# Kernel tuning notes

Hardware: AMD Instinct MI355X
Metric: run time of the kernel (lower is better)

The kernel has to match this reference:

```python
import jax, jax.numpy as jnp
import numpy as np
import math

B, T, D = 4, 4096, 512
K_CACHE = 16

def _layernorm(x, g, b, eps=1e-5):
    mu = x.mean(-1, keepdims=True)
    var = ((x - mu) ** 2).mean(-1, keepdims=True)
    return (x - mu) / jnp.sqrt(var + eps) * g + b

def _shift1(x):
    # prepend zero along time axis, drop last: x_prev[t] = x[t-1]
    return jnp.pad(x, ((0, 0), (1, 0), (0, 0)))[:, :-1]

def mipt_parallel_scan(p, theta, inp_re, inp_im):
    # Faithful replication of the torch loop: ceil(log2(T+1)) iterations,
    # each combining with the element shifted by ONE position (as written).
    Bt, Tt, Dt = p.shape
    a_re = (1.0 - p) * jnp.cos(theta)
    a_im = (1.0 - p) * jnp.sin(theta)
    b_re, b_im = inp_re, inp_im
    mask = (jnp.arange(Tt) >= 1)[None, :, None]
    steps = math.ceil(math.log2(Tt + 1))
    for _ in range(steps):
        ar_p, ai_p = _shift1(a_re), _shift1(a_im)
        br_p, bi_p = _shift1(b_re), _shift1(b_im)
        new_a_re = a_re * ar_p - a_im * ai_p
        new_a_im = a_re * ai_p + a_im * ar_p
        new_b_re = a_re * br_p - a_im * bi_p + b_re
        new_b_im = a_re * bi_p + a_im * br_p + b_im
        a_re = jnp.where(mask, new_a_re, a_re)
        a_im = jnp.where(mask, new_a_im, a_im)
        b_re = jnp.where(mask, new_b_re, b_re)
        b_im = jnp.where(mask, new_b_im, b_im)
    return b_re, b_im

def setup_inputs() -> dict:
    key = jax.random.key(0)
    ks = jax.random.split(key, 32)
    s = 0.02
    def W(k, i, o):
        return jax.random.normal(k, (i, o), jnp.float32) * s
    inp = {
        'x': jax.random.normal(ks[0], (B, T, D), jnp.float32),
        'ln1_g': jnp.ones((D,), jnp.float32), 'ln1_b': jnp.zeros((D,), jnp.float32),
        'ln2_g': jnp.ones((D,), jnp.float32), 'ln2_b': jnp.zeros((D,), jnp.float32),
        'Wp_w': W(ks[1], D, D), 'Wp_b': jnp.zeros((D,), jnp.float32),
        'Wt_w': W(ks[2], D, D), 'Wt_b': jnp.zeros((D,), jnp.float32),
        'Wr_w': W(ks[3], D, D), 'Wr_b': jnp.zeros((D,), jnp.float32),
        'Wi_w': W(ks[4], D, D), 'Wi_b': jnp.zeros((D,), jnp.float32),
        'Wk_w': W(ks[5], D, D), 'Wk_b': jnp.zeros((D,), jnp.float32),
        'Wv_w': W(ks[6], D, D), 'Wv_b': jnp.zeros((D,), jnp.float32),
        'Wq_w': W(ks[7], D, D), 'Wq_b': jnp.zeros((D,), jnp.float32),
        'gate_w': W(ks[8], D, 1), 'gate_b': jnp.zeros((1,), jnp.float32),
        'ffn1_w': W(ks[9], D, 4 * D), 'ffn1_b': jnp.zeros((4 * D,), jnp.float32),
        'ffn2_w': W(ks[10], 4 * D, D), 'ffn2_b': jnp.zeros((D,), jnp.float32),
    }
    return inp

def reference(x, ln1_g, ln1_b, ln2_g, ln2_b, Wp_w, Wp_b, Wt_w, Wt_b, Wr_w, Wr_b,
              Wi_w, Wi_b, Wk_w, Wk_b, Wv_w, Wv_b, Wq_w, Wq_b, gate_w, gate_b,
              ffn1_w, ffn1_b, ffn2_w, ffn2_b):
    Bx, Tx, Dx = x.shape
    residual = x
    xn = _layernorm(x, ln1_g, ln1_b)
    p = jax.nn.sigmoid(xn @ Wp_w + Wp_b)
    theta = xn @ Wt_w + Wt_b
    inp_re = xn @ Wr_w + Wr_b
    inp_im = xn @ Wi_w + Wi_b
    h_re, _h_im = mipt_parallel_scan(p, theta, inp_re, inp_im)
    h_mean = h_re.mean(axis=1)  # [B, D]
    # CausalSparseCache (eval mode)
    p_scalar = p.mean(axis=-1)  # [B, T]
    K = min(K_CACHE, Tx)
    _, topk_idx = jax.lax.top_k(p_scalar, K)  # [B, K]
    idx = jnp.broadcast_to(topk_idx[:, :, None], (Bx, K, Dx))
    h_topk = jnp.take_along_axis(h_re, idx, axis=1)  # [B, K, D]
    keys = h_topk @ Wk_w + Wk_b
    values = h_topk @ Wv_w + Wv_b
    query = (h_mean @ Wq_w + Wq_b)[:, None, :]  # [B, 1, D]
    scores = jnp.einsum('bqd,bkd->bqk', query, keys) / math.sqrt(Dx)
    attn = jax.nn.softmax(scores, axis=-1)
    cache_out = jnp.einsum('bqk,bkd->bqd', attn, values)[:, 0]  # [B, D]
    g = jax.nn.sigmoid(h_mean @ gate_w + gate_b)  # [B, 1]
    out = h_mean + g * cache_out
    h = h_re + residual
    hn = _layernorm(h, ln2_g, ln2_b)
    ffn = jax.nn.gelu(hn @ ffn1_w + ffn1_b, approximate=False) @ ffn2_w + ffn2_b
    h = h + ffn
    return (h, out)
```

## Files before the change

### kernel.cpp

```cpp
#include <hip/hip_runtime.h>
#include <hip/hip_bf16.h>
#include <cstdint>
#include <cstddef>

typedef __bf16 bf16;
typedef __attribute__((ext_vector_type(8))) __bf16 bf16x8;
typedef __attribute__((ext_vector_type(4))) __bf16 bf16x4;
typedef __attribute__((ext_vector_type(4))) float f32x4;

#define BB 4
#define TT 4096
#define DD 512
#define MM (BB * TT)
#define OUT1_OFF ((size_t)MM * DD)

typedef __attribute__((address_space(1))) void as1_void;
typedef __attribute__((address_space(3))) void as3_void;

__device__ __forceinline__ void gl_lds16(const void* g, void* l) {
    __builtin_amdgcn_global_load_lds((as1_void*)(uintptr_t)g,
                                     (as3_void*)(uintptr_t)l, 16, 0, 0);
}

#define SIGM(x) (__builtin_amdgcn_rcpf(1.f + __expf(-(x))))

__global__ void transpose_bf16(const float* __restrict__ in, bf16* __restrict__ out,
                               int R, int C) {
    __shared__ float tile[32][33];
    const int c0 = blockIdx.x * 32, r0 = blockIdx.y * 32;
    const int tx = threadIdx.x, ty = threadIdx.y;
#pragma unroll
    for (int i = 0; i < 32; i += 8)
        tile[ty + i][tx] = in[(size_t)(r0 + ty + i) * C + (c0 + tx)];
    __syncthreads();
#pragma unroll
    for (int i = 0; i < 32; i += 8)
        out[(size_t)(c0 + ty + i) * R + (r0 + tx)] = (bf16)tile[tx][ty + i];
}

__global__ void pack_bias(const float* __restrict__ a, const float* __restrict__ b,
                          const float* __restrict__ c, const float* __restrict__ d,
                          float* __restrict__ o) {
    const int i = blockIdx.x * 256 + threadIdx.x;
    if (i < 2048) {
        const float* s = (i < 512) ? a : (i < 1024) ? b : (i < 1536) ? c : d;
        o[i] = s[i & 511];
    }
}

__global__ void zero_kernel(float* __restrict__ p, int n) {
    const int i = blockIdx.x * 256 + threadIdx.x;
    if (i < n) p[i] = 0.f;
}

__global__ __launch_bounds__(256) void ln_kernel(
    const float* __restrict__ X, const float* __restrict__ Xadd,
    const float* __restrict__ gw, const float* __restrict__ bw,
    bf16* __restrict__ out) {
    const int row = blockIdx.x * 4 + (threadIdx.x >> 6);
    const int lane = threadIdx.x & 63;
    const float* xr = X + (size_t)row * DD + lane * 8;
    float v[8];
    float4 v0 = *(const float4*)xr;
    float4 v1 = *(const float4*)(xr + 4);
    v[0] = v0.x; v[1] = v0.y; v[2] = v0.z; v[3] = v0.w;
    v[4] = v1.x; v[5] = v1.y; v[6] = v1.z; v[7] = v1.w;
    if (Xadd) {
        const float* ad = Xadd + (size_t)row * DD + lane * 8;
        float4 a0 = *(const float4*)ad;
        float4 a1 = *(const float4*)(ad + 4);
        v[0] += a0.x; v[1] += a0.y; v[2] += a0.z; v[3] += a0.w;
        v[4] += a1.x; v[5] += a1.y; v[6] += a1.z; v[7] += a1.w;
    }
    float s = 0.f, ss = 0.f;
#pragma unroll
    for (int i = 0; i < 8; ++i) { s += v[i]; ss += v[i] * v[i]; }
#pragma unroll
    for (int o = 32; o; o >>= 1) { s += __shfl_down(s, o); ss += __shfl_down(ss, o); }
    s = __shfl(s, 0); ss = __shfl(ss, 0);
    const float mu = s * (1.f / DD);
    const float var = ss * (1.f / DD) - mu * mu;
    const float rstd = rsqrtf(var + 1e-5f);
    bf16x8 o8;
#pragma unroll
    for (int i = 0; i < 8; ++i)
        o8[i] = (bf16)((v[i] - mu) * rstd * gw[lane * 8 + i] + bw[lane * 8 + i]);
    *(bf16x8*)(out + (size_t)row * DD + lane * 8) = o8;
}

#define MF(a_, b_, c_) c_ = __builtin_amdgcn_mfma_f32_16x16x32_bf16(a_, b_, c_, 0, 0, 0)

template <int MODE>
__global__ __launch_bounds__(256) void gemm_bt(
    const bf16* __restrict__ A, const bf16* __restrict__ Bt,
    const float* __restrict__ bias, void* __restrict__ Cout,
    void* __restrict__ Cout2,
    const float* __restrict__ add1, const float* __restrict__ add2,
    int M, int N, int K) {
    __shared__ bf16 As[3][4096];
    __shared__ bf16 Bs[3][4096];
    const int tid = threadIdx.x;
    const int lane = tid & 63;
    const int wv = tid >> 6;
    const int wr = wv >> 1, wc = wv & 1;
    const int nb = N >> 7;
    const int nwg = gridDim.x;
    int bx = blockIdx.x;
    if ((nwg & 7) == 0) bx = (bx & 7) * (nwg >> 3) + (bx >> 3);
    const int bm = bx / nb, bn = bx % nb;
    const int m0 = bm << 7, n0 = bn << 7;

    const int srow = tid >> 2;
    const int scol = (((tid & 3) ^ ((tid >> 3) & 3)) << 3);
    const bf16* Asrc = A + (size_t)(m0 + srow) * K + scol;
    const bf16* Bsrc = Bt + (size_t)(n0 + srow) * K + scol;
    const size_t rstep = (size_t)64 * K;

    const int lr = lane & 15, lg = lane >> 4;
    const int sel = ((lg ^ ((lr >> 1) & 3)) << 3);
    const int aoff = (wr * 64 + lr) * 32 + sel;
    const int boff = (wc * 64 + lr) * 32 + sel;

#define STG(buf, k0)                                                \
    do {                                                            \
        gl_lds16(Asrc + (k0),         &As[buf][wv * 512]);          \
        gl_lds16(Asrc + (k0) + rstep, &As[buf][wv * 512 + 2048]);   \
        gl_lds16(Bsrc + (k0),         &Bs[buf][wv * 512]);          \
        gl_lds16(Bsrc + (k0) + rstep, &Bs[buf][wv * 512 + 2048]);   \
    } while (0)

    f32x4 acc00 = {}, acc01 = {}, acc02 = {}, acc03 = {};
    f32x4 acc10 = {}, acc11 = {}, acc12 = {}, acc13 = {};
    f32x4 acc20 = {}, acc21 = {}, acc22 = {}, acc23 = {};
    f32x4 acc30 = {}, acc31 = {}, acc32 = {}, acc33 = {};

    const int NT = K >> 5;
    STG(0, 0);
    STG(1, 32);
    int cur = 0;
    for (int t = 0; t < NT; ++t) {
        if (t + 1 < NT) asm volatile("s_waitcnt vmcnt(4)" ::: "memory");
        else            asm volatile("s_waitcnt vmcnt(0)" ::: "memory");
        __builtin_amdgcn_s_barrier();
        asm volatile("" ::: "memory");
        const bf16* Ab = As[cur];
        const bf16* Bb = Bs[cur];
        bf16x8 af0 = *(const bf16x8*)&Ab[aoff];
        bf16x8 af1 = *(const bf16x8*)&Ab[aoff + 512];
        bf16x8 af2 = *(const bf16x8*)&Ab[aoff + 1024];
        bf16x8 af3 = *(const bf16x8*)&Ab[aoff + 1536];
        bf16x8 bf0 = *(const bf16x8*)&Bb[boff];
        bf16x8 bf1 = *(const bf16x8*)&Bb[boff + 512];
        bf16x8 bf2 = *(const bf16x8*)&Bb[boff + 1024];
        bf16x8 bf3 = *(const bf16x8*)&Bb[boff + 1536];
        if (t + 2 < NT) {
            const int stg = (cur == 0) ? 2 : cur - 1;
            STG(stg, (t + 2) << 5);
        }
        MF(af0, bf0, acc00); MF(af0, bf1, acc01); MF(af0, bf2, acc02); MF(af0, bf3, acc03);
        MF(af1, bf0, acc10); MF(af1, bf1, acc11); MF(af1, bf2, acc12); MF(af1, bf3, acc13);
        MF(af2, bf0, acc20); MF(af2, bf1, acc21); MF(af2, bf2, acc22); MF(af2, bf3, acc23);
        MF(af3, bf0, acc30); MF(af3, bf1, acc31); MF(af3, bf2, acc32); MF(af3, bf3, acc33);
        cur = (cur == 2) ? 0 : cur + 1;
    }
#undef STG

    if constexpr (MODE == 0) {
        const int cls = n0 >> 9;
        if (cls == 0) {
            const int pidx = (n0 + wc * 64) >> 6;
#define EPI0(mi, A0, A1, A2, A3)                                              \
    do {                                                                      \
        const int gmb = m0 + wr * 64 + mi * 16 + 4 * lg;                      \
        const int dbase = n0 + wc * 64 + lr;                                  \
        const float b0_ = bias[dbase], b1_ = bias[dbase + 16],                \
                    b2_ = bias[dbase + 32], b3_ = bias[dbase + 48];           \
        _Pragma("unroll")                                                     \
        for (int i = 0; i < 4; ++i) {                                         \
            const int row = gmb + i;                                          \
            const float p0 = SIGM(A0[i] + b0_);                               \
            const float p1 = SIGM(A1[i] + b1_);                               \
            const float p2 = SIGM(A2[i] + b2_);                               \
            const float p3 = SIGM(A3[i] + b3_);                               \
            bf16* ob = (bf16*)Cout + (size_t)row * 2048;                      \
            ob[(size_t)dbase * 4]        = (bf16)(1.f - p0);                  \
            ob[(size_t)(dbase + 16) * 4] = (bf16)(1.f - p1);                  \
            ob[(size_t)(dbase + 32) * 4] = (bf16)(1.f - p2);                  \
            ob[(size_t)(dbase + 48) * 4] = (bf16)(1.f - p3);                  \
            float s_ = p0 + p1 + p2 + p3;                                     \
            s_ += __shfl_xor(s_, 1); s_ += __shfl_xor(s_, 2);                 \
            s_ += __shfl_xor(s_, 4); s_ += __shfl_xor(s_, 8);                 \
            if (lr == 0) ((float*)Cout2)[(size_t)pidx * MM + row] = s_;       \
        }                                                                     \
    } while (0)
            EPI0(0, acc00, acc01, acc02, acc03);
            EPI0(1, acc10, acc11, acc12, acc13);
            EPI0(2, acc20, acc21, acc22, acc23);
            EPI0(3, acc30, acc31, acc32, acc33);
#undef EPI0
        } else {
#define EPIS(mi, ni, ACC)                                                     \
    do {                                                                      \
        const int gmb = m0 + wr * 64 + mi * 16 + 4 * lg;                      \
        const int gn = n0 + wc * 64 + ni * 16 + lr;                           \
        const int dn = gn & 511;                                              \
        const float bia = bias[gn];                                           \
        _Pragma("unroll")                                                     \
        for (int i = 0; i < 4; ++i)                                           \
            ((bf16*)Cout)[((size_t)(gmb + i) * 512 + dn) * 4 + cls] =         \
                (bf16)(ACC[i] + bia);                                         \
    } while (0)
            EPIS(0, 0, acc00); EPIS(0, 1, acc01); EPIS(0, 2, acc02); EPIS(0, 3, acc03);
            EPIS(1, 0, acc10); EPIS(1, 1, acc11); EPIS(1, 2, acc12); EPIS(1, 3, acc13);
            EPIS(2, 0, acc20); EPIS(2, 1, acc21); EPIS(2, 2, acc22); EPIS(2, 3, acc23);
            EPIS(3, 0, acc30); EPIS(3, 1, acc31); EPIS(3, 2, acc32); EPIS(3, 3, acc33);
#undef EPIS
        }
    } else {
#define EPI(mi, ni, ACC)                                                        \
    do {                                                                        \
        const int gmb = m0 + wr * 64 + mi * 16 + 4 * lg;                        \
        const int gn = n0 + wc * 64 + ni * 16 + lr;                             \
        const float bia = bias[gn];                                             \
        _Pragma("unroll")                                                       \
        for (int i = 0; i < 4; ++i) {                                           \
            float v = ACC[i] + bia;                                             \
            const int row = gmb + i;                                            \
            if (MODE == 1) {                                                    \
                const float ge = 0.5f * v * (1.0f + erff(v * 0.70710678118654752f)); \
                ((bf16*)Cout)[(size_t)row * N + gn] = (bf16)ge;                 \
            } else {                                                            \
                const size_t off = (size_t)row * N + gn;                        \
                ((float*)Cout)[off] = v + add1[off] + add2[off];                \
            }                                                                   \
        }                                                                       \
    } while (0)
        EPI(0, 0, acc00); EPI(0, 1, acc01); EPI(0, 2, acc02); EPI(0, 3, acc03);
        EPI(1, 0, acc10); EPI(1, 1, acc11); EPI(1, 2, acc12); EPI(1, 3, acc13);
        EPI(2, 0, acc20); EPI(2, 1, acc21); EPI(2, 2, acc22); EPI(2, 3, acc23);
        EPI(3, 0, acc30); EPI(3, 1, acc31); EPI(3, 2, acc32); EPI(3, 3, acc33);
#undef EPI
    }
}

__global__ __launch_bounds__(256) void pscalar_fin(const float* __restrict__ part,
                                                   float* __restrict__ ps) {
    const int i = blockIdx.x * 256 + threadIdx.x;
    float s = 0.f;
#pragma unroll
    for (int j = 0; j < 8; ++j) s += part[(size_t)j * MM + i];
    ps[i] = s * (1.f / 512.f);
}

#define SCL 32
__global__ __launch_bounds__(256) void scan_kernel(const bf16* __restrict__ lint4,
                                                   float* __restrict__ h_re,
                                                   float* __restrict__ hsum) {
    const int blk = blockIdx.x;
    const int dh = blk & 1;
    const int tc = (blk >> 1) & 127;
    const int b = blk >> 8;
    const int d = dh * 256 + threadIdx.x;
    const int t0 = tc * SCL;

    float par[13], pai[13], pbr[13], pbi[13];
#pragma unroll
    for (int k = 0; k < 13; ++k) { par[k] = 0.f; pai[k] = 0.f; pbr[k] = 0.f; pbi[k] = 0.f; }

    const int warm = (tc == 0) ? 0 : 13;
    const bf16* tp = lint4 + ((size_t)(b * TT + t0 - warm) * 512 + d) * 4;
    float* pout = h_re + ((size_t)(b * TT + t0)) * DD + d;

#define XFORM(car, cai, cbr, cbi)                                        \
    const bf16x4 q_ = *(const bf16x4*)tp;                                \
    tp += 2048;                                                          \
    const float om = (float)q_[0];                                       \
    const float th = (float)q_[1];                                       \
    const float cbr = (float)q_[2];                                      \
    const float cbi = (float)q_[3];                                      \
    float fr_, sn, cs;                                                   \
    { const float rv_ = th * 0.15915494309189535f;                       \
      asm("v_fract_f32 %0, %1" : "=v"(fr_) : "v"(rv_));                  \
      asm("v_sin_f32 %0, %1" : "=v"(sn) : "v"(fr_));                     \
      asm("v_cos_f32 %0, %1" : "=v"(cs) : "v"(fr_)); }                   \
    float car = om * cs, cai = om * sn;

    for (int s = 0; s < warm; ++s) {
        XFORM(car, cai, cbr, cbi)
        float br_ = cbr, bi_ = cbi;
#pragma unroll
        for (int k = 0; k < 13; ++k) {
            const float tar = par[k], tai = pai[k], tbr = pbr[k], tbi = pbi[k];
            par[k] = car; pai[k] = cai; pbr[k] = br_; pbi[k] = bi_;
            const float nbr = car * tbr - cai * tbi + br_;
            const float nbi = car * tbi + cai * tbr + bi_;
            if (k < 12) {
                const float nar = car * tar - cai * tai;
                const float nai = car * tai + cai * tar;
                car = nar; cai = nai;
            }
            br_ = nbr; bi_ = nbi;
        }
    }

    float hacc = 0.f;
#pragma unroll 4
    for (int s = 0; s < SCL; ++s) {
        const int t = t0 + s;
        XFORM(car, cai, cbr, cbi)
        float br_ = cbr, bi_ = cbi;
        if (t == 0) {
#pragma unroll
            for (int k = 0; k < 13; ++k) { par[k] = car; pai[k] = cai; pbr[k] = br_; pbi[k] = bi_; }
        } else {
#pragma unroll
            for (int k = 0; k < 13; ++k) {
                const float tar = par[k], tai = pai[k], tbr = pbr[k], tbi = pbi[k];
                par[k] = car; pai[k] = cai; pbr[k] = br_; pbi[k] = bi_;
                const float nbr = car * tbr - cai * tbi + br_;
                const float nbi = car * tbi + cai * tbr + bi_;
                if (k < 12) {
                    const float nar = car * tar - cai * tai;
                    const float nai = car * tai + cai * tar;
                    car = nar; cai = nai;
                }
                br_ = nbr; bi_ = nbi;
            }
        }
        pout[(size_t)s * DD] = br_;
        hacc += br_;
    }
#undef XFORM
    atomicAdd(&hsum[b * DD + d], hacc);
}

__global__ __launch_bounds__(256) void topk_kernel(const float* __restrict__ ps,
                                                   int* __restrict__ idx_out) {
    __shared__ float vals[TT];
    __shared__ float rv[4];
    __shared__ int ri[4];
    const int b = blockIdx.x, tid = threadIdx.x;
    for (int i = tid; i < TT; i += 256) vals[i] = ps[b * TT + i];
    __syncthreads();
    for (int kk = 0; kk < 16; ++kk) {
        float bv = -1e30f; int bi = 0x7fffffff;
        for (int i = tid; i < TT; i += 256) {
            const float v = vals[i];
            if (v > bv || (v == bv && i < bi)) { bv = v; bi = i; }
        }
#pragma unroll
        for (int o = 32; o; o >>= 1) {
            const float ov = __shfl_down(bv, o);
            const int oi = __shfl_down(bi, o);
            if (ov > bv || (ov == bv && oi < bi)) { bv = ov; bi = oi; }
        }
        const int lane = tid & 63, wid = tid >> 6;
        if (!lane) { rv[wid] = bv; ri[wid] = bi; }
        __syncthreads();
        if (!tid) {
            float fbv = rv[0]; int fbi = ri[0];
            for (int w = 1; w < 4; ++w)
                if (rv[w] > fbv || (rv[w] == fbv && ri[w] < fbi)) { fbv = rv[w]; fbi = ri[w]; }
            idx_out[b * 16 + kk] = fbi;
            vals[fbi] = -1e30f;
        }
        __syncthreads();
    }
}

__global__ __launch_bounds__(256) void kv_kernel(
    const float* __restrict__ h_re, const int* __restrict__ tki,
    const float* __restrict__ Wk, const float* __restrict__ Wkb,
    const float* __restrict__ Wv, const float* __restrict__ Wvb,
    float* __restrict__ keys, float* __restrict__ vals) {
    const int blk = blockIdx.x;
    const int b = blk >> 4, j = blk & 15;
    const int tid = threadIdx.x;
    __shared__ float hrow[512];
    const int row = tki[b * 16 + j];
    for (int i = tid; i < 512; i += 256)
        hrow[i] = h_re[((size_t)(b * TT + row)) * DD + i];
    __syncthreads();
    for (int n = tid; n < 512; n += 256) {
        float sk = Wkb[n], sv = Wvb[n];
        for (int k = 0; k < 512; ++k) {
            const float h = hrow[k];
            sk += h * Wk[(size_t)k * 512 + n];
            sv += h * Wv[(size_t)k * 512 + n];
        }
        keys[((size_t)(b * 16 + j)) * 512 + n] = sk;
        vals[((size_t)(b * 16 + j)) * 512 + n] = sv;
    }
}

__global__ __launch_bounds__(256) void attn_out_kernel(
    const float* __restrict__ hsum, const float* __restrict__ Wq,
    const float* __restrict__ Wqb, const float* __restrict__ gw,
    const float* __restrict__ gb, const float* __restrict__ keys,
    const float* __restrict__ vals, float* __restrict__ out1) {
    const int b = blockIdx.x, tid = threadIdx.x;
    const int lane = tid & 63, wid = tid >> 6;
    __shared__ float hm[512];
    __shared__ float q[512];
    __shared__ float sc[16];
    __shared__ float red[4];
    for (int d0 = tid; d0 < 512; d0 += 256)
        hm[d0] = hsum[b * 512 + d0] * (1.f / 4096.f);
    __syncthreads();
    for (int n = tid; n < 512; n += 256) {
        float s = Wqb[n];
        for (int k = 0; k < 512; ++k) s += hm[k] * Wq[(size_t)k * 512 + n];
        q[n] = s;
    }
    float gp = 0.f;
    for (int k = tid; k < 512; k += 256) gp += hm[k] * gw[k];
#pragma unroll
    for (int o = 32; o; o >>= 1) gp += __shfl_down(gp, o);
    if (!lane) red[wid] = gp;
    __syncthreads();
    const float g = 1.f / (1.f + __expf(-(red[0] + red[1] + red[2] + red[3] + gb[0])));
    for (int kk = wid; kk < 16; kk += 4) {
        float sp = 0.f;
        const float* kr = keys + ((size_t)(b * 16 + kk)) * 512;
        for (int k2 = lane; k2 < 512; k2 += 64) sp += q[k2] * kr[k2];
#pragma unroll
        for (int o = 32; o; o >>= 1) sp += __shfl_down(sp, o);
        if (!lane) sc[kk] = sp * 0.04419417382415922f;
    }
    __syncthreads();
    float mx = sc[0];
#pragma unroll
    for (int kk = 1; kk < 16; ++kk) mx = fmaxf(mx, sc[kk]);
    float den = 0.f;
    float w16[16];
#pragma unroll
    for (int kk = 0; kk < 16; ++kk) { w16[kk] = __expf(sc[kk] - mx); den += w16[kk]; }
    const float rden = 1.f / den;
    for (int d0 = tid; d0 < 512; d0 += 256) {
        float co = 0.f;
#pragma unroll
        for (int kk = 0; kk < 16; ++kk)
            co += w16[kk] * vals[((size_t)(b * 16 + kk)) * 512 + d0];
        out1[b * 512 + d0] = hm[d0] + g * (co * rden);
    }
}

extern "C" void kernel_launch(void* const* d_in, const int* in_sizes, int n_in,
                              void* d_out, int out_size, void* d_ws, size_t ws_size,
                              hipStream_t stream) {
    const float* x    = (const float*)d_in[0];
    const float* ln1g = (const float*)d_in[1];
    const float* ln1b = (const float*)d_in[2];
    const float* ln2g = (const float*)d_in[3];
    const float* ln2b = (const float*)d_in[4];
    const float* Wp_w = (const float*)d_in[5];
    const float* Wp_b = (const float*)d_in[6];
    const float* Wt_w = (const float*)d_in[7];
    const float* Wt_b = (const float*)d_in[8];
    const float* Wr_w = (const float*)d_in[9];
    const float* Wr_b = (const float*)d_in[10];
    const float* Wi_w = (const float*)d_in[11];
    const float* Wi_b = (const float*)d_in[12];
    const float* Wk_w = (const float*)d_in[13];
    const float* Wk_b = (const float*)d_in[14];
    const float* Wv_w = (const float*)d_in[15];
    const float* Wv_b = (const float*)d_in[16];
    const float* Wq_w = (const float*)d_in[17];
    const float* Wq_b = (const float*)d_in[18];
    const float* gw   = (const float*)d_in[19];
    const float* gb   = (const float*)d_in[20];
    const float* f1w  = (const float*)d_in[21];
    const float* f1b  = (const float*)d_in[22];
    const float* f2w  = (const float*)d_in[23];
    const float* f2b  = (const float*)d_in[24];

    char* wsp = (char*)d_ws;
    bf16* lint4 = (bf16*)wsp;
    char* p = wsp + 67108864;
    float* h_re = (float*)p; p += 33554432;
    bf16* xn = (bf16*)p;     p += 16777216;
    bf16* hn = (bf16*)p;     p += 16777216;
    bf16* wcat = (bf16*)p;   p += 2097152;
    bf16* f1bt = (bf16*)p;   p += 2097152;
    bf16* f2bt = (bf16*)p;   p += 2097152;
    float* bcat = (float*)p; p += 8192;
    float* ps = (float*)p;   p += 65536;
    float* pspart = (float*)p; p += 524288;
    float* hsum = (float*)p; p += 8192;
    int* tki = (int*)p;      p += 256;
    float* keys = (float*)p; p += 131072;
    float* valsb = (float*)p;
    bf16* act = (bf16*)wsp;
    float* out0 = (float*)d_out;
    float* out1 = (float*)d_out + OUT1_OFF;

    dim3 tb(32, 8);
    transpose_bf16<<<dim3(16, 16), tb, 0, stream>>>(Wp_w, wcat + (size_t)0 * 512 * 512, 512, 512);
    transpose_bf16<<<dim3(16, 16), tb, 0, stream>>>(Wt_w, wcat + (size_t)1 * 512 * 512, 512, 512);
    transpose_bf16<<<dim3(16, 16), tb, 0, stream>>>(Wr_w, wcat + (size_t)2 * 512 * 512, 512, 512);
    transpose_bf16<<<dim3(16, 16), tb, 0, stream>>>(Wi_w, wcat + (size_t)3 * 512 * 512, 512, 512);
    transpose_bf16<<<dim3(64, 16), tb, 0, stream>>>(f1w, f1bt, 512, 2048);
    transpose_bf16<<<dim3(16, 64), tb, 0, stream>>>(f2w, f2bt, 2048, 512);
    pack_bias<<<8, 256, 0, stream>>>(Wp_b, Wt_b, Wr_b, Wi_b, bcat);

    ln_kernel<<<4096, 256, 0, stream>>>(x, nullptr, ln1g, ln1b, xn);
    gemm_bt<0><<<2048, 256, 0, stream>>>(xn, wcat, bcat, lint4, pspart, nullptr, nullptr, MM, 2048, 512);
    pscalar_fin<<<64, 256, 0, stream>>>(pspart, ps);
    zero_kernel<<<8, 256, 0, stream>>>(hsum, 2048);
    scan_kernel<<<1024, 256, 0, stream>>>(lint4, h_re, hsum);
    topk_kernel<<<4, 256, 0, stream>>>(ps, tki);
    kv_kernel<<<64, 256, 0, stream>>>(h_re, tki, Wk_w, Wk_b, Wv_w, Wv_b, keys, valsb);
    attn_out_kernel<<<4, 256, 0, stream>>>(hsum, Wq_w, Wq_b, gw, gb, keys, valsb, out1);
    ln_kernel<<<4096, 256, 0, stream>>>(h_re, x, ln2g, ln2b, hn);
    gemm_bt<1><<<2048, 256, 0, stream>>>(hn, f1bt, f1b, act, nullptr, nullptr, nullptr, MM, 2048, 512);
    gemm_bt<2><<<512, 256, 0, stream>>>(act, f2bt, f2b, out0, nullptr, h_re, x, MM, 512, 2048);
}
```

Measured before the change: 409.6 us.

## Use single-wave 64x64 GEMM tiles for K=512 GEMMs and interleave two scan chunks

Adds a one-wave-per-block GEMM with 64x64 tiles and a 3-stage global-to-LDS pipeline. It is used for the fused projection GEMM and the FFN1 GEMM, which gives 8192 small blocks instead of 2048 four-wave blocks, removing block-level barriers and exposing more parallel blocks. Each scan thread now processes two interleaved 32-step chunks, halving the grid and giving independent instruction streams to hide latency. The cost is redundant warmup work and more registers per scan thread, plus halved operand reuse per tile in the GEMMs.

```diff
diff --git a/kernel.cpp b/kernel.cpp
--- a/kernel.cpp
+++ b/kernel.cpp
@@ -91,10 +91,136 @@
 #define MF(a_, b_, c_) c_ = __builtin_amdgcn_mfma_f32_16x16x32_bf16(a_, b_, c_, 0, 0, 0)
 
 template <int MODE>
+__global__ __launch_bounds__(64) void gemm_wv(
+    const bf16* __restrict__ A, const bf16* __restrict__ Bt,
+    const float* __restrict__ bias, void* __restrict__ Cout,
+    void* __restrict__ Cout2, int M, int N, int K) {
+    __shared__ bf16 As[3][2048];
+    __shared__ bf16 Bs[3][2048];
+    const int lane = threadIdx.x;
+    const int nb = N >> 6;
+    const int nwg = gridDim.x;
+    int bx = blockIdx.x;
+    if ((nwg & 7) == 0) bx = (bx & 7) * (nwg >> 3) + (bx >> 3);
+    const int bm = bx / nb, bn = bx % nb;
+    const int m0 = bm << 6, n0 = bn << 6;
+
+    const int srow = lane >> 2;
+    const int scol = (((lane & 3) ^ ((lane >> 3) & 3)) << 3);
+    const bf16* Asrc = A + (size_t)(m0 + srow) * K + scol;
+    const bf16* Bsrc = Bt + (size_t)(n0 + srow) * K + scol;
+    const size_t rs16 = (size_t)16 * K;
+
+    const int lr = lane & 15, lg = lane >> 4;
+    const int sel = ((lg ^ ((lr >> 1) & 3)) << 3);
+    const int fbase = lr * 32 + sel;
+
+#define STGW(buf, k0)                                          \
+    do {                                                       \
+        gl_lds16(Asrc + (k0),              &As[buf][0]);       \
+        gl_lds16(Asrc + (k0) + rs16,       &As[buf][512]);     \
+        gl_lds16(Asrc + (k0) + 2 * rs16,   &As[buf][1024]);    \
+        gl_lds16(Asrc + (k0) + 3 * rs16,   &As[buf][1536]);    \
+        gl_lds16(Bsrc + (k0),              &Bs[buf][0]);       \
+        gl_lds16(Bsrc + (k0) + rs16,       &Bs[buf][512]);     \
+        gl_lds16(Bsrc + (k0) + 2 * rs16,   &Bs[buf][1024]);    \
+        gl_lds16(Bsrc + (k0) + 3 * rs16,   &Bs[buf][1536]);    \
+    } while (0)
+
+    f32x4 acc[4][4] = {};
+    const int NT = K >> 5;
+    STGW(0, 0);
+    STGW(1, 32);
+    int cur = 0;
+    for (int t = 0; t < NT; ++t) {
+        if (t + 1 < NT) asm volatile("s_waitcnt vmcnt(8)" ::: "memory");
+        else            asm volatile("s_waitcnt vmcnt(0)" ::: "memory");
+        const bf16* Ab = As[cur];
+        const bf16* Bb = Bs[cur];
+        bf16x8 af[4], bfv[4];
+#pragma unroll
+        for (int mi = 0; mi < 4; ++mi) af[mi] = *(const bf16x8*)&Ab[fbase + mi * 512];
+#pragma unroll
+        for (int ni = 0; ni < 4; ++ni) bfv[ni] = *(const bf16x8*)&Bb[fbase + ni * 512];
+        if (t + 2 < NT) {
+            const int stg = (cur == 0) ? 2 : cur - 1;
+            STGW(stg, (t + 2) << 5);
+        }
+#pragma unroll
+        for (int mi = 0; mi < 4; ++mi)
+#pragma unroll
+            for (int ni = 0; ni < 4; ++ni)
+                acc[mi][ni] = __builtin_amdgcn_mfma_f32_16x16x32_bf16(
+                    af[mi], bfv[ni], acc[mi][ni], 0, 0, 0);
+        cur = (cur == 2) ? 0 : cur + 1;
+    }
+#undef STGW
+
+    if constexpr (MODE == 0) {
+        const int cls = n0 >> 9;
+        if (cls == 0) {
+            const int pidx = n0 >> 6;
+#pragma unroll
+            for (int mi = 0; mi < 4; ++mi) {
+                const int gmb = m0 + mi * 16 + 4 * lg;
+                const int dbase = n0 + lr;
+                const float b0_ = bias[dbase], b1_ = bias[dbase + 16],
+                            b2_ = bias[dbase + 32], b3_ = bias[dbase + 48];
+#pragma unroll
+                for (int i = 0; i < 4; ++i) {
+                    const int row = gmb + i;
+                    const float p0 = SIGM(acc[mi][0][i] + b0_);
+                    const float p1 = SIGM(acc[mi][1][i] + b1_);
+                    const float p2 = SIGM(acc[mi][2][i] + b2_);
+                    const float p3 = SIGM(acc[mi][3][i] + b3_);
+                    bf16* ob = (bf16*)Cout + (size_t)row * 2048;
+                    ob[(size_t)dbase * 4]        = (bf16)(1.f - p0);
+                    ob[(size_t)(dbase + 16) * 4] = (bf16)(1.f - p1);
+                    ob[(size_t)(dbase + 32) * 4] = (bf16)(1.f - p2);
+                    ob[(size_t)(dbase + 48) * 4] = (bf16)(1.f - p3);
+                    float s_ = p0 + p1 + p2 + p3;
+                    s_ += __shfl_xor(s_, 1); s_ += __shfl_xor(s_, 2);
+                    s_ += __shfl_xor(s_, 4); s_ += __shfl_xor(s_, 8);
+                    if (lr == 0) ((float*)Cout2)[(size_t)pidx * MM + row] = s_;
+                }
+            }
+        } else {
+#pragma unroll
+            for (int mi = 0; mi < 4; ++mi)
+#pragma unroll
+                for (int ni = 0; ni < 4; ++ni) {
+                    const int gmb = m0 + mi * 16 + 4 * lg;
+                    const int gn = n0 + ni * 16 + lr;
+                    const int dn = gn & 511;
+                    const float bia = bias[gn];
+#pragma unroll
+                    for (int i = 0; i < 4; ++i)
+                        ((bf16*)Cout)[((size_t)(gmb + i) * 512 + dn) * 4 + cls] =
+                            (bf16)(acc[mi][ni][i] + bia);
+                }
+        }
+    } else {
+#pragma unroll
+        for (int mi = 0; mi < 4; ++mi)
+#pragma unroll
+            for (int ni = 0; ni < 4; ++ni) {
+                const int gmb = m0 + mi * 16 + 4 * lg;
+                const int gn = n0 + ni * 16 + lr;
+                const float bia = bias[gn];
+#pragma unroll
+                for (int i = 0; i < 4; ++i) {
+                    const float v = acc[mi][ni][i] + bia;
+                    const float ge = 0.5f * v * (1.0f + erff(v * 0.70710678118654752f));
+                    ((bf16*)Cout)[(size_t)(gmb + i) * N + gn] = (bf16)ge;
+                }
+            }
+    }
+}
+
+template <int MODE>
 __global__ __launch_bounds__(256) void gemm_bt(
     const bf16* __restrict__ A, const bf16* __restrict__ Bt,
     const float* __restrict__ bias, void* __restrict__ Cout,
-    void* __restrict__ Cout2,
     const float* __restrict__ add1, const float* __restrict__ add2,
     int M, int N, int K) {
     __shared__ bf16 As[3][4096];
@@ -165,58 +291,6 @@
     }
 #undef STG
 
-    if constexpr (MODE == 0) {
-        const int cls = n0 >> 9;
-        if (cls == 0) {
-            const int pidx = (n0 + wc * 64) >> 6;
-#define EPI0(mi, A0, A1, A2, A3)                                              \
-    do {                                                                      \
-        const int gmb = m0 + wr * 64 + mi * 16 + 4 * lg;                      \
-        const int dbase = n0 + wc * 64 + lr;                                  \
-        const float b0_ = bias[dbase], b1_ = bias[dbase + 16],                \
-                    b2_ = bias[dbase + 32], b3_ = bias[dbase + 48];           \
-        _Pragma("unroll")                                                     \
-        for (int i = 0; i < 4; ++i) {                                         \
-            const int row = gmb + i;                                          \
-            const float p0 = SIGM(A0[i] + b0_);                               \
-            const float p1 = SIGM(A1[i] + b1_);                               \
-            const float p2 = SIGM(A2[i] + b2_);                               \
-            const float p3 = SIGM(A3[i] + b3_);                               \
-            bf16* ob = (bf16*)Cout + (size_t)row * 2048;                      \
-            ob[(size_t)dbase * 4]        = (bf16)(1.f - p0);                  \
-            ob[(size_t)(dbase + 16) * 4] = (bf16)(1.f - p1);                  \
-            ob[(size_t)(dbase + 32) * 4] = (bf16)(1.f - p2);                  \
-            ob[(size_t)(dbase + 48) * 4] = (bf16)(1.f - p3);                  \
-            float s_ = p0 + p1 + p2 + p3;                                     \
-            s_ += __shfl_xor(s_, 1); s_ += __shfl_xor(s_, 2);                 \
-            s_ += __shfl_xor(s_, 4); s_ += __shfl_xor(s_, 8);                 \
-            if (lr == 0) ((float*)Cout2)[(size_t)pidx * MM + row] = s_;       \
-        }                                                                     \
-    } while (0)
-            EPI0(0, acc00, acc01, acc02, acc03);
-            EPI0(1, acc10, acc11, acc12, acc13);
-            EPI0(2, acc20, acc21, acc22, acc23);
-            EPI0(3, acc30, acc31, acc32, acc33);
-#undef EPI0
-        } else {
-#define EPIS(mi, ni, ACC)                                                     \
-    do {                                                                      \
-        const int gmb = m0 + wr * 64 + mi * 16 + 4 * lg;                      \
-        const int gn = n0 + wc * 64 + ni * 16 + lr;                           \
-        const int dn = gn & 511;                                              \
-        const float bia = bias[gn];                                           \
-        _Pragma("unroll")                                                     \
-        for (int i = 0; i < 4; ++i)                                           \
-            ((bf16*)Cout)[((size_t)(gmb + i) * 512 + dn) * 4 + cls] =         \
-                (bf16)(ACC[i] + bia);                                         \
-    } while (0)
-            EPIS(0, 0, acc00); EPIS(0, 1, acc01); EPIS(0, 2, acc02); EPIS(0, 3, acc03);
-            EPIS(1, 0, acc10); EPIS(1, 1, acc11); EPIS(1, 2, acc12); EPIS(1, 3, acc13);
-            EPIS(2, 0, acc20); EPIS(2, 1, acc21); EPIS(2, 2, acc22); EPIS(2, 3, acc23);
-            EPIS(3, 0, acc30); EPIS(3, 1, acc31); EPIS(3, 2, acc32); EPIS(3, 3, acc33);
-#undef EPIS
-        }
-    } else {
 #define EPI(mi, ni, ACC)                                                        \
     do {                                                                        \
         const int gmb = m0 + wr * 64 + mi * 16 + 4 * lg;                        \
@@ -225,22 +299,15 @@
         _Pragma("unroll")                                                       \
         for (int i = 0; i < 4; ++i) {                                           \
             float v = ACC[i] + bia;                                             \
-            const int row = gmb + i;                                            \
-            if (MODE == 1) {                                                    \
-                const float ge = 0.5f * v * (1.0f + erff(v * 0.70710678118654752f)); \
-                ((bf16*)Cout)[(size_t)row * N + gn] = (bf16)ge;                 \
-            } else {                                                            \
-                const size_t off = (size_t)row * N + gn;                        \
-                ((float*)Cout)[off] = v + add1[off] + add2[off];                \
-            }                                                                   \
+            const size_t off = (size_t)(gmb + i) * N + gn;                      \
+            ((float*)Cout)[off] = v + add1[off] + add2[off];                    \
         }                                                                       \
     } while (0)
-        EPI(0, 0, acc00); EPI(0, 1, acc01); EPI(0, 2, acc02); EPI(0, 3, acc03);
-        EPI(1, 0, acc10); EPI(1, 1, acc11); EPI(1, 2, acc12); EPI(1, 3, acc13);
-        EPI(2, 0, acc20); EPI(2, 1, acc21); EPI(2, 2, acc22); EPI(2, 3, acc23);
-        EPI(3, 0, acc30); EPI(3, 1, acc31); EPI(3, 2, acc32); EPI(3, 3, acc33);
+    EPI(0, 0, acc00); EPI(0, 1, acc01); EPI(0, 2, acc02); EPI(0, 3, acc03);
+    EPI(1, 0, acc10); EPI(1, 1, acc11); EPI(1, 2, acc12); EPI(1, 3, acc13);
+    EPI(2, 0, acc20); EPI(2, 1, acc21); EPI(2, 2, acc22); EPI(2, 3, acc23);
+    EPI(3, 0, acc30); EPI(3, 1, acc31); EPI(3, 2, acc32); EPI(3, 3, acc33);
 #undef EPI
-    }
 }
 
 __global__ __launch_bounds__(256) void pscalar_fin(const float* __restrict__ part,
@@ -253,86 +320,94 @@
 }
 
 #define SCL 32
+#define STAGE13(par, pai, pbr, pbi, car, cai, br_, bi_)                     \
+    _Pragma("unroll")                                                       \
+    for (int k = 0; k < 13; ++k) {                                          \
+        const float tar = par[k], tai = pai[k], tbr = pbr[k], tbi = pbi[k]; \
+        par[k] = car; pai[k] = cai; pbr[k] = br_; pbi[k] = bi_;             \
+        const float nbr = car * tbr - cai * tbi + br_;                      \
+        const float nbi = car * tbi + cai * tbr + bi_;                      \
+        if (k < 12) {                                                       \
+            const float nar = car * tar - cai * tai;                        \
+            const float nai = car * tai + cai * tar;                        \
+            car = nar; cai = nai;                                           \
+        }                                                                   \
+        br_ = nbr; bi_ = nbi;                                               \
+    }
+
+#define XF(tp, car, cai, br_, bi_)                                       \
+    {                                                                    \
+        const bf16x4 q_ = *(const bf16x4*)(tp);                          \
+        (tp) += 2048;                                                    \
+        const float om_ = (float)q_[0];                                  \
+        const float th_ = (float)q_[1];                                  \
+        br_ = (float)q_[2];                                              \
+        bi_ = (float)q_[3];                                              \
+        float fr_, sn_, cs_;                                             \
+        const float rv_ = th_ * 0.15915494309189535f;                    \
+        asm("v_fract_f32 %0, %1" : "=v"(fr_) : "v"(rv_));                \
+        asm("v_sin_f32 %0, %1" : "=v"(sn_) : "v"(fr_));                  \
+        asm("v_cos_f32 %0, %1" : "=v"(cs_) : "v"(fr_));                  \
+        car = om_ * cs_; cai = om_ * sn_;                                \
+    }
+
 __global__ __launch_bounds__(256) void scan_kernel(const bf16* __restrict__ lint4,
                                                    float* __restrict__ h_re,
                                                    float* __restrict__ hsum) {
     const int blk = blockIdx.x;
-    const int dh = blk & 1;
-    const int tc = (blk >> 1) & 127;
-    const int b = blk >> 8;
+    const int b = blk >> 7;
+    const int rem = blk & 127;
+    const int dh = rem & 1;
+    const int tcp = rem >> 1;
     const int d = dh * 256 + threadIdx.x;
-    const int t0 = tc * SCL;
-
-    float par[13], pai[13], pbr[13], pbi[13];
-#pragma unroll
-    for (int k = 0; k < 13; ++k) { par[k] = 0.f; pai[k] = 0.f; pbr[k] = 0.f; pbi[k] = 0.f; }
-
-    const int warm = (tc == 0) ? 0 : 13;
-    const bf16* tp = lint4 + ((size_t)(b * TT + t0 - warm) * 512 + d) * 4;
-    float* pout = h_re + ((size_t)(b * TT + t0)) * DD + d;
-
-#define XFORM(car, cai, cbr, cbi)                                        \
-    const bf16x4 q_ = *(const bf16x4*)tp;                                \
-    tp += 2048;                                                          \
-    const float om = (float)q_[0];                                       \
-    const float th = (float)q_[1];                                       \
-    const float cbr = (float)q_[2];                                      \
-    const float cbi = (float)q_[3];                                      \
-    float fr_, sn, cs;                                                   \
-    { const float rv_ = th * 0.15915494309189535f;                       \
-      asm("v_fract_f32 %0, %1" : "=v"(fr_) : "v"(rv_));                  \
-      asm("v_sin_f32 %0, %1" : "=v"(sn) : "v"(fr_));                     \
-      asm("v_cos_f32 %0, %1" : "=v"(cs) : "v"(fr_)); }                   \
-    float car = om * cs, cai = om * sn;
-
-    for (int s = 0; s < warm; ++s) {
-        XFORM(car, cai, cbr, cbi)
-        float br_ = cbr, bi_ = cbi;
-#pragma unroll
-        for (int k = 0; k < 13; ++k) {
-            const float tar = par[k], tai = pai[k], tbr = pbr[k], tbi = pbi[k];
-            par[k] = car; pai[k] = cai; pbr[k] = br_; pbi[k] = bi_;
-            const float nbr = car * tbr - cai * tbi + br_;
-            const float nbi = car * tbi + cai * tbr + bi_;
-            if (k < 12) {
-                const float nar = car * tar - cai * tai;
-                const float nai = car * tai + cai * tar;
-                car = nar; cai = nai;
-            }
-            br_ = nbr; bi_ = nbi;
-        }
+    const int t0a = tcp * 64;
+    const int t0b = t0a + 32;
+
+    float parA[13], paiA[13], pbrA[13], pbiA[13];
+    float parB[13], paiB[13], pbrB[13], pbiB[13];
+#pragma unroll
+    for (int k = 0; k < 13; ++k) {
+        parA[k] = 0.f; paiA[k] = 0.f; pbrA[k] = 0.f; pbiA[k] = 0.f;
+        parB[k] = 0.f; paiB[k] = 0.f; pbrB[k] = 0.f; pbiB[k] = 0.f;
+    }
+
+    const int warmA = (tcp == 0) ? 0 : 13;
+    const bf16* tpA = lint4 + ((size_t)(b * TT + t0a - warmA) * 512 + d) * 4;
+    const bf16* tpB = lint4 + ((size_t)(b * TT + t0b - 13) * 512 + d) * 4;
+    float* poutA = h_re + ((size_t)(b * TT + t0a)) * DD + d;
+    float* poutB = h_re + ((size_t)(b * TT + t0b)) * DD + d;
+
+    float carA, caiA, brA, biA, carB, caiB, brB, biB;
+    for (int s = 0; s < 13; ++s) {
+        if (tcp != 0) {
+            XF(tpA, carA, caiA, brA, biA)
+            STAGE13(parA, paiA, pbrA, pbiA, carA, caiA, brA, biA)
+        }
+        XF(tpB, carB, caiB, brB, biB)
+        STAGE13(parB, paiB, pbrB, pbiB, carB, caiB, brB, biB)
     }
 
     float hacc = 0.f;
-#pragma unroll 4
+#pragma unroll 2
     for (int s = 0; s < SCL; ++s) {
-        const int t = t0 + s;
-        XFORM(car, cai, cbr, cbi)
-        float br_ = cbr, bi_ = cbi;
-        if (t == 0) {
-#pragma unroll
-            for (int k = 0; k < 13; ++k) { par[k] = car; pai[k] = cai; pbr[k] = br_; pbi[k] = bi_; }
+        XF(tpA, carA, caiA, brA, biA)
+        if (tcp == 0 && s == 0) {
+#pragma unroll
+            for (int k = 0; k < 13; ++k) { parA[k] = carA; paiA[k] = caiA; pbrA[k] = brA; pbiA[k] = biA; }
         } else {
-#pragma unroll
-            for (int k = 0; k < 13; ++k) {
-                const float tar = par[k], tai = pai[k], tbr = pbr[k], tbi = pbi[k];
-                par[k] = car; pai[k] = cai; pbr[k] = br_; pbi[k] = bi_;
-                const float nbr = car * tbr - cai * tbi + br_;
-                const float nbi = car * tbi + cai * tbr + bi_;
-                if (k < 12) {
-                    const float nar = car * tar - cai * tai;
-                    const float nai = car * tai + cai * tar;
-                    car = nar; cai = nai;
-                }
-                br_ = nbr; bi_ = nbi;
-            }
-        }
-        pout[(size_t)s * DD] = br_;
-        hacc += br_;
-    }
-#undef XFORM
+            STAGE13(parA, paiA, pbrA, pbiA, carA, caiA, brA, biA)
+        }
+        poutA[(size_t)s * DD] = brA;
+        hacc += brA;
+        XF(tpB, carB, caiB, brB, biB)
+        STAGE13(parB, paiB, pbrB, pbiB, carB, caiB, brB, biB)
+        poutB[(size_t)s * DD] = brB;
+        hacc += brB;
+    }
     atomicAdd(&hsum[b * DD + d], hacc);
 }
+#undef XF
+#undef STAGE13
 
 __global__ __launch_bounds__(256) void topk_kernel(const float* __restrict__ ps,
                                                    int* __restrict__ idx_out) {
@@ -504,14 +579,14 @@
     pack_bias<<<8, 256, 0, stream>>>(Wp_b, Wt_b, Wr_b, Wi_b, bcat);
 
     ln_kernel<<<4096, 256, 0, stream>>>(x, nullptr, ln1g, ln1b, xn);
-    gemm_bt<0><<<2048, 256, 0, stream>>>(xn, wcat, bcat, lint4, pspart, nullptr, nullptr, MM, 2048, 512);
+    gemm_wv<0><<<8192, 64, 0, stream>>>(xn, wcat, bcat, lint4, pspart, MM, 2048, 512);
     pscalar_fin<<<64, 256, 0, stream>>>(pspart, ps);
     zero_kernel<<<8, 256, 0, stream>>>(hsum, 2048);
-    scan_kernel<<<1024, 256, 0, stream>>>(lint4, h_re, hsum);
+    scan_kernel<<<512, 256, 0, stream>>>(lint4, h_re, hsum);
     topk_kernel<<<4, 256, 0, stream>>>(ps, tki);
     kv_kernel<<<64, 256, 0, stream>>>(h_re, tki, Wk_w, Wk_b, Wv_w, Wv_b, keys, valsb);
     attn_out_kernel<<<4, 256, 0, stream>>>(hsum, Wq_w, Wq_b, gw, gb, keys, valsb, out1);
     ln_kernel<<<4096, 256, 0, stream>>>(h_re, x, ln2g, ln2b, hn);
-    gemm_bt<1><<<2048, 256, 0, stream>>>(hn, f1bt, f1b, act, nullptr, nullptr, nullptr, MM, 2048, 512);
-    gemm_bt<2><<<512, 256, 0, stream>>>(act, f2bt, f2b, out0, nullptr, h_re, x, MM, 512, 2048);
-}
+    gemm_wv<1><<<8192, 64, 0, stream>>>(hn, f1bt, f1b, act, nullptr, MM, 2048, 512);
+    gemm_bt<2><<<512, 256, 0, stream>>>(act, f2bt, f2b, out0, h_re, x, MM, 512, 2048);
+}
```

New measurement: 458.0 us. 1.12x slower.

## Store scan output h_re in bf16 and process two time chunks per scan thread

Applied to the files above, without the earlier changes.

The intermediate h_re buffer goes from fp32 to bf16. This halves its write traffic in the scan and its reads in kv, ln2 and the FFN2 epilogue residual. The scan kernel now handles two interleaved 32-step chunks per thread with half as many blocks, giving two independent dependency chains for more instruction-level parallelism. In exchange h_re loses precision, which feeds both the residual output and the top-k cache path, and each scan thread uses more registers.

```diff
diff --git a/kernel.cpp b/kernel.cpp
--- a/kernel.cpp
+++ b/kernel.cpp
@@ -54,7 +54,7 @@
 }
 
 __global__ __launch_bounds__(256) void ln_kernel(
-    const float* __restrict__ X, const float* __restrict__ Xadd,
+    const float* __restrict__ X, const bf16* __restrict__ Xadd,
     const float* __restrict__ gw, const float* __restrict__ bw,
     bf16* __restrict__ out) {
     const int row = blockIdx.x * 4 + (threadIdx.x >> 6);
@@ -66,11 +66,9 @@
     v[0] = v0.x; v[1] = v0.y; v[2] = v0.z; v[3] = v0.w;
     v[4] = v1.x; v[5] = v1.y; v[6] = v1.z; v[7] = v1.w;
     if (Xadd) {
-        const float* ad = Xadd + (size_t)row * DD + lane * 8;
-        float4 a0 = *(const float4*)ad;
-        float4 a1 = *(const float4*)(ad + 4);
-        v[0] += a0.x; v[1] += a0.y; v[2] += a0.z; v[3] += a0.w;
-        v[4] += a1.x; v[5] += a1.y; v[6] += a1.z; v[7] += a1.w;
+        const bf16x8 a8 = *(const bf16x8*)(Xadd + (size_t)row * DD + lane * 8);
+#pragma unroll
+        for (int i = 0; i < 8; ++i) v[i] += (float)a8[i];
     }
     float s = 0.f, ss = 0.f;
 #pragma unroll
@@ -95,7 +93,7 @@
     const bf16* __restrict__ A, const bf16* __restrict__ Bt,
     const float* __restrict__ bias, void* __restrict__ Cout,
     void* __restrict__ Cout2,
-    const float* __restrict__ add1, const float* __restrict__ add2,
+    const bf16* __restrict__ add1, const float* __restrict__ add2,
     int M, int N, int K) {
     __shared__ bf16 As[3][4096];
     __shared__ bf16 Bs[3][4096];
@@ -231,7 +229,7 @@
                 ((bf16*)Cout)[(size_t)row * N + gn] = (bf16)ge;                 \
             } else {                                                            \
                 const size_t off = (size_t)row * N + gn;                        \
-                ((float*)Cout)[off] = v + add1[off] + add2[off];                \
+                ((float*)Cout)[off] = v + (float)add1[off] + add2[off];         \
             }                                                                   \
         }                                                                       \
     } while (0)
@@ -253,86 +251,94 @@
 }
 
 #define SCL 32
+#define STAGE13(par, pai, pbr, pbi, car, cai, br_, bi_)                     \
+    _Pragma("unroll")                                                       \
+    for (int k = 0; k < 13; ++k) {                                          \
+        const float tar = par[k], tai = pai[k], tbr = pbr[k], tbi = pbi[k]; \
+        par[k] = car; pai[k] = cai; pbr[k] = br_; pbi[k] = bi_;             \
+        const float nbr = car * tbr - cai * tbi + br_;                      \
+        const float nbi = car * tbi + cai * tbr + bi_;                      \
+        if (k < 12) {                                                       \
+            const float nar = car * tar - cai * tai;                        \
+            const float nai = car * tai + cai * tar;                        \
+            car = nar; cai = nai;                                           \
+        }                                                                   \
+        br_ = nbr; bi_ = nbi;                                               \
+    }
+
+#define XF(tp, car, cai, br_, bi_)                                       \
+    {                                                                    \
+        const bf16x4 q_ = *(const bf16x4*)(tp);                          \
+        (tp) += 2048;                                                    \
+        const float om_ = (float)q_[0];                                  \
+        const float th_ = (float)q_[1];                                  \
+        br_ = (float)q_[2];                                              \
+        bi_ = (float)q_[3];                                              \
+        float fr_, sn_, cs_;                                             \
+        const float rv_ = th_ * 0.15915494309189535f;                    \
+        asm("v_fract_f32 %0, %1" : "=v"(fr_) : "v"(rv_));                \
+        asm("v_sin_f32 %0, %1" : "=v"(sn_) : "v"(fr_));                  \
+        asm("v_cos_f32 %0, %1" : "=v"(cs_) : "v"(fr_));                  \
+        car = om_ * cs_; cai = om_ * sn_;                                \
+    }
+
 __global__ __launch_bounds__(256) void scan_kernel(const bf16* __restrict__ lint4,
-                                                   float* __restrict__ h_re,
+                                                   bf16* __restrict__ h_re,
                                                    float* __restrict__ hsum) {
     const int blk = blockIdx.x;
-    const int dh = blk & 1;
-    const int tc = (blk >> 1) & 127;
-    const int b = blk >> 8;
+    const int b = blk >> 7;
+    const int rem = blk & 127;
+    const int dh = rem & 1;
+    const int tcp = rem >> 1;
     const int d = dh * 256 + threadIdx.x;
-    const int t0 = tc * SCL;
-
-    float par[13], pai[13], pbr[13], pbi[13];
-#pragma unroll
-    for (int k = 0; k < 13; ++k) { par[k] = 0.f; pai[k] = 0.f; pbr[k] = 0.f; pbi[k] = 0.f; }
-
-    const int warm = (tc == 0) ? 0 : 13;
-    const bf16* tp = lint4 + ((size_t)(b * TT + t0 - warm) * 512 + d) * 4;
-    float* pout = h_re + ((size_t)(b * TT + t0)) * DD + d;
-
-#define XFORM(car, cai, cbr, cbi)                                        \
-    const bf16x4 q_ = *(const bf16x4*)tp;                                \
-    tp += 2048;                                                          \
-    const float om = (float)q_[0];                                       \
-    const float th = (float)q_[1];                                       \
-    const float cbr = (float)q_[2];                                      \
-    const float cbi = (float)q_[3];                                      \
-    float fr_, sn, cs;                                                   \
-    { const float rv_ = th * 0.15915494309189535f;                       \
-      asm("v_fract_f32 %0, %1" : "=v"(fr_) : "v"(rv_));                  \
-      asm("v_sin_f32 %0, %1" : "=v"(sn) : "v"(fr_));                     \
-      asm("v_cos_f32 %0, %1" : "=v"(cs) : "v"(fr_)); }                   \
-    float car = om * cs, cai = om * sn;
-
-    for (int s = 0; s < warm; ++s) {
-        XFORM(car, cai, cbr, cbi)
-        float br_ = cbr, bi_ = cbi;
-#pragma unroll
-        for (int k = 0; k < 13; ++k) {
-            const float tar = par[k], tai = pai[k], tbr = pbr[k], tbi = pbi[k];
-            par[k] = car; pai[k] = cai; pbr[k] = br_; pbi[k] = bi_;
-            const float nbr = car * tbr - cai * tbi + br_;
-            const float nbi = car * tbi + cai * tbr + bi_;
-            if (k < 12) {
-                const float nar = car * tar - cai * tai;
-                const float nai = car * tai + cai * tar;
-                car = nar; cai = nai;
-            }
-            br_ = nbr; bi_ = nbi;
-        }
+    const int t0a = tcp * 64;
+    const int t0b = t0a + 32;
+
+    float parA[13], paiA[13], pbrA[13], pbiA[13];
+    float parB[13], paiB[13], pbrB[13], pbiB[13];
+#pragma unroll
+    for (int k = 0; k < 13; ++k) {
+        parA[k] = 0.f; paiA[k] = 0.f; pbrA[k] = 0.f; pbiA[k] = 0.f;
+        parB[k] = 0.f; paiB[k] = 0.f; pbrB[k] = 0.f; pbiB[k] = 0.f;
+    }
+
+    const int warmA = (tcp == 0) ? 0 : 13;
+    const bf16* tpA = lint4 + ((size_t)(b * TT + t0a - warmA) * 512 + d) * 4;
+    const bf16* tpB = lint4 + ((size_t)(b * TT + t0b - 13) * 512 + d) * 4;
+    bf16* poutA = h_re + ((size_t)(b * TT + t0a)) * DD + d;
+    bf16* poutB = h_re + ((size_t)(b * TT + t0b)) * DD + d;
+
+    float carA, caiA, brA, biA, carB, caiB, brB, biB;
+    for (int s = 0; s < 13; ++s) {
+        if (tcp != 0) {
+            XF(tpA, carA, caiA, brA, biA)
+            STAGE13(parA, paiA, pbrA, pbiA, carA, caiA, brA, biA)
+        }
+        XF(tpB, carB, caiB, brB, biB)
+        STAGE13(parB, paiB, pbrB, pbiB, carB, caiB, brB, biB)
     }
 
     float hacc = 0.f;
-#pragma unroll 4
+#pragma unroll 2
     for (int s = 0; s < SCL; ++s) {
-        const int t = t0 + s;
-        XFORM(car, cai, cbr, cbi)
-        float br_ = cbr, bi_ = cbi;
-        if (t == 0) {
-#pragma unroll
-            for (int k = 0; k < 13; ++k) { par[k] = car; pai[k] = cai; pbr[k] = br_; pbi[k] = bi_; }
+        XF(tpA, carA, caiA, brA, biA)
+        if (tcp == 0 && s == 0) {
+#pragma unroll
+            for (int k = 0; k < 13; ++k) { parA[k] = carA; paiA[k] = caiA; pbrA[k] = brA; pbiA[k] = biA; }
         } else {
-#pragma unroll
-            for (int k = 0; k < 13; ++k) {
-                const float tar = par[k], tai = pai[k], tbr = pbr[k], tbi = pbi[k];
-                par[k] = car; pai[k] = cai; pbr[k] = br_; pbi[k] = bi_;
-                const float nbr = car * tbr - cai * tbi + br_;
-                const float nbi = car * tbi + cai * tbr + bi_;
-                if (k < 12) {
-                    const float nar = car * tar - cai * tai;
-                    const float nai = car * tai + cai * tar;
-                    car = nar; cai = nai;
-                }
-                br_ = nbr; bi_ = nbi;
-            }
-        }
-        pout[(size_t)s * DD] = br_;
-        hacc += br_;
-    }
-#undef XFORM
+            STAGE13(parA, paiA, pbrA, pbiA, carA, caiA, brA, biA)
+        }
+        poutA[(size_t)s * DD] = (bf16)brA;
+        hacc += brA;
+        XF(tpB, carB, caiB, brB, biB)
+        STAGE13(parB, paiB, pbrB, pbiB, carB, caiB, brB, biB)
+        poutB[(size_t)s * DD] = (bf16)brB;
+        hacc += brB;
+    }
     atomicAdd(&hsum[b * DD + d], hacc);
 }
+#undef XF
+#undef STAGE13
 
 __global__ __launch_bounds__(256) void topk_kernel(const float* __restrict__ ps,
                                                    int* __restrict__ idx_out) {
@@ -369,7 +375,7 @@
 }
 
 __global__ __launch_bounds__(256) void kv_kernel(
-    const float* __restrict__ h_re, const int* __restrict__ tki,
+    const bf16* __restrict__ h_re, const int* __restrict__ tki,
     const float* __restrict__ Wk, const float* __restrict__ Wkb,
     const float* __restrict__ Wv, const float* __restrict__ Wvb,
     float* __restrict__ keys, float* __restrict__ vals) {
@@ -379,7 +385,7 @@
     __shared__ float hrow[512];
     const int row = tki[b * 16 + j];
     for (int i = tid; i < 512; i += 256)
-        hrow[i] = h_re[((size_t)(b * TT + row)) * DD + i];
+        hrow[i] = (float)h_re[((size_t)(b * TT + row)) * DD + i];
     __syncthreads();
     for (int n = tid; n < 512; n += 256) {
         float sk = Wkb[n], sv = Wvb[n];
@@ -477,7 +483,7 @@
     char* wsp = (char*)d_ws;
     bf16* lint4 = (bf16*)wsp;
     char* p = wsp + 67108864;
-    float* h_re = (float*)p; p += 33554432;
+    bf16* h_re = (bf16*)p;   p += 16777216;
     bf16* xn = (bf16*)p;     p += 16777216;
     bf16* hn = (bf16*)p;     p += 16777216;
     bf16* wcat = (bf16*)p;   p += 2097152;
@@ -507,11 +513,11 @@
     gemm_bt<0><<<2048, 256, 0, stream>>>(xn, wcat, bcat, lint4, pspart, nullptr, nullptr, MM, 2048, 512);
     pscalar_fin<<<64, 256, 0, stream>>>(pspart, ps);
     zero_kernel<<<8, 256, 0, stream>>>(hsum, 2048);
-    scan_kernel<<<1024, 256, 0, stream>>>(lint4, h_re, hsum);
+    scan_kernel<<<512, 256, 0, stream>>>(lint4, h_re, hsum);
     topk_kernel<<<4, 256, 0, stream>>>(ps, tki);
     kv_kernel<<<64, 256, 0, stream>>>(h_re, tki, Wk_w, Wk_b, Wv_w, Wv_b, keys, valsb);
     attn_out_kernel<<<4, 256, 0, stream>>>(hsum, Wq_w, Wq_b, gw, gb, keys, valsb, out1);
-    ln_kernel<<<4096, 256, 0, stream>>>(h_re, x, ln2g, ln2b, hn);
+    ln_kernel<<<4096, 256, 0, stream>>>(x, h_re, ln2g, ln2b, hn);
     gemm_bt<1><<<2048, 256, 0, stream>>>(hn, f1bt, f1b, act, nullptr, nullptr, nullptr, MM, 2048, 512);
     gemm_bt<2><<<512, 256, 0, stream>>>(act, f2bt, f2b, out0, nullptr, h_re, x, MM, 512, 2048);
 }
```

Result: no change. 404.8 us (-1.2%).
